# Performance work log

Measured on AMD Instinct MI355X. Metric: run time of the kernel, lower is better.

The kernel has to match this reference:

```python
import jax, jax.numpy as jnp
import numpy as np

SINGLE_DIM = 256
PAIR_DIM = 64
MAX_REL_POS = 32
LN_EPS = 1e-5


def setup_inputs() -> dict:
    key = jax.random.key(0)
    ks = jax.random.split(key, 6)
    B, N = 2, 1024
    single_repr = jax.random.normal(ks[0], (B, N, SINGLE_DIM), dtype=jnp.float32)
    # Linear(single_dim*2 -> pair_dim)
    lim = 1.0 / np.sqrt(2 * SINGLE_DIM)
    W = jax.random.uniform(ks[1], (2 * SINGLE_DIM, PAIR_DIM), minval=-lim, maxval=lim, dtype=jnp.float32)
    b = jax.random.uniform(ks[2], (PAIR_DIM,), minval=-lim, maxval=lim, dtype=jnp.float32)
    # LayerNorm(pair_dim)
    gamma = jnp.ones((PAIR_DIM,), dtype=jnp.float32)
    beta = jnp.zeros((PAIR_DIM,), dtype=jnp.float32)
    # Embedding(2*max_rel_pos+1, pair_dim)
    embed = jax.random.normal(ks[3], (2 * MAX_REL_POS + 1, PAIR_DIM), dtype=jnp.float32)
    return {"single_repr": single_repr, "W": W, "b": b, "gamma": gamma, "beta": beta, "embed": embed}


def reference(single_repr, W, b, gamma, beta, embed):
    B, N, d = single_repr.shape
    # Split the Linear weight: cat([s_i, s_j]) @ W == s_i @ W_i + s_j @ W_j.
    # This avoids materializing the [B,N,N,2d] concat tensor (outer-sum trick).
    W_i, W_j = W[:d], W[d:]                       # [d, pair_dim] each
    proj_i = jnp.einsum('bnd,dp->bnp', single_repr, W_i)  # [B,N,P]
    proj_j = jnp.einsum('bnd,dp->bnp', single_repr, W_j)  # [B,N,P]
    x = proj_i[:, :, None, :] + proj_j[:, None, :, :] + b  # [B,N,N,P]
    # LayerNorm over last dim
    mu = jnp.mean(x, axis=-1, keepdims=True)
    var = jnp.mean((x - mu) ** 2, axis=-1, keepdims=True)
    x = (x - mu) * jax.lax.rsqrt(var + LN_EPS) * gamma + beta
    x = jax.nn.relu(x)
    # Relative position embedding
    pos = jnp.arange(N)
    rel = jnp.clip(pos[None, :] - pos[:, None], -MAX_REL_POS, MAX_REL_POS) + MAX_REL_POS  # [N,N]
    x = x + embed[rel][None]  # broadcast over batch
    return x
```

## Files before the change

### kernel.cpp

```cpp
#include <hip/hip_runtime.h>

#define SINGLE_DIM 256
#define PAIR_DIM   64
#define MAX_REL    32
#define LN_EPS     1e-5f
#define N_FIXED    1024

__global__ __launch_bounds__(128) void proj_kernel(
    const float* __restrict__ s,
    const float* __restrict__ W,
    const float* __restrict__ bias,
    float* __restrict__ proj)
{
    __shared__ float lds[4][SINGLE_DIM];
    const int row0 = blockIdx.x * 4;
    const int t = threadIdx.x;

    {
        const float4* src = (const float4*)(s + (size_t)row0 * SINGLE_DIM);
        float4* dst = (float4*)(&lds[0][0]);
        dst[t]       = src[t];
        dst[t + 128] = src[t + 128];
    }
    __syncthreads();

    const int c4   = (t & 31) * 4;
    const int row  = t >> 5;
    const int half = c4 >> 6;
    const int p0   = c4 & 63;
    const float* Wbase = W + half * (SINGLE_DIM * PAIR_DIM) + p0;
    const float* srow  = lds[row];

    float4 acc = {0.f, 0.f, 0.f, 0.f};
    #pragma unroll
    for (int d = 0; d < SINGLE_DIM; d += 4) {
        float4 s4 = *(const float4*)(srow + d);
        float4 w0 = *(const float4*)(Wbase + (d + 0) * PAIR_DIM);
        float4 w1 = *(const float4*)(Wbase + (d + 1) * PAIR_DIM);
        float4 w2 = *(const float4*)(Wbase + (d + 2) * PAIR_DIM);
        float4 w3 = *(const float4*)(Wbase + (d + 3) * PAIR_DIM);
        acc.x += s4.x * w0.x; acc.y += s4.x * w0.y; acc.z += s4.x * w0.z; acc.w += s4.x * w0.w;
        acc.x += s4.y * w1.x; acc.y += s4.y * w1.y; acc.z += s4.y * w1.z; acc.w += s4.y * w1.w;
        acc.x += s4.z * w2.x; acc.y += s4.z * w2.y; acc.z += s4.z * w2.z; acc.w += s4.z * w2.w;
        acc.x += s4.w * w3.x; acc.y += s4.w * w3.y; acc.z += s4.w * w3.z; acc.w += s4.w * w3.w;
    }
    if (half == 0) {
        float4 b4 = *(const float4*)(bias + p0);
        acc.x += b4.x; acc.y += b4.y; acc.z += b4.z; acc.w += b4.w;
    }
    *(float4*)(proj + (size_t)(row0 + row) * 128 + c4) = acc;
}

__global__ __launch_bounds__(256) void pair_kernel(
    const float* __restrict__ proj,
    const float* __restrict__ gamma,
    const float* __restrict__ beta,
    const float* __restrict__ embed,
    float* __restrict__ out)
{
    const int t = threadIdx.x;
    const int pairIdx = blockIdx.x * 16 + (t >> 4);
    const int p0 = (t & 15) * 4;

    const int j  = pairIdx & (N_FIXED - 1);
    const int bi = pairIdx >> 10;
    const int i  = bi & (N_FIXED - 1);
    const int b  = bi >> 10;

    const float4 pi4 = *(const float4*)(proj + (size_t)bi * 128 + p0);
    const float4 pj4 = *(const float4*)(proj + (size_t)(b * N_FIXED + j) * 128 + 64 + p0);

    float4 v;
    v.x = pi4.x + pj4.x;
    v.y = pi4.y + pj4.y;
    v.z = pi4.z + pj4.z;
    v.w = pi4.w + pj4.w;

    float s  = v.x + v.y + v.z + v.w;
    float ss = v.x * v.x + v.y * v.y + v.z * v.z + v.w * v.w;
    #pragma unroll
    for (int mask = 1; mask < 16; mask <<= 1) {
        s  += __shfl_xor(s,  mask, 64);
        ss += __shfl_xor(ss, mask, 64);
    }
    const float mean = s * (1.f / PAIR_DIM);
    const float var  = ss * (1.f / PAIR_DIM) - mean * mean;
    const float rstd = rsqrtf(var + LN_EPS);

    const float4 g4 = *(const float4*)(gamma + p0);
    const float4 b4 = *(const float4*)(beta + p0);

    int rel = j - i;
    rel = (rel < -MAX_REL) ? -MAX_REL : (rel > MAX_REL ? MAX_REL : rel);
    rel += MAX_REL;
    const float4 e4 = *(const float4*)(embed + rel * PAIR_DIM + p0);

    float4 o;
    o.x = fmaxf((v.x - mean) * rstd * g4.x + b4.x, 0.f) + e4.x;
    o.y = fmaxf((v.y - mean) * rstd * g4.y + b4.y, 0.f) + e4.y;
    o.z = fmaxf((v.z - mean) * rstd * g4.z + b4.z, 0.f) + e4.z;
    o.w = fmaxf((v.w - mean) * rstd * g4.w + b4.w, 0.f) + e4.w;

    *(float4*)(out + (size_t)pairIdx * PAIR_DIM + p0) = o;
}

extern "C" void kernel_launch(void* const* d_in, const int* in_sizes, int n_in,
                              void* d_out, int out_size, void* d_ws, size_t ws_size,
                              hipStream_t stream) {
    const float* s     = (const float*)d_in[0];
    const float* W     = (const float*)d_in[1];
    const float* bias  = (const float*)d_in[2];
    const float* gamma = (const float*)d_in[3];
    const float* beta  = (const float*)d_in[4];
    const float* embed = (const float*)d_in[5];
    float* out  = (float*)d_out;
    float* proj = (float*)d_ws;

    const int BN = in_sizes[0] / SINGLE_DIM;

    proj_kernel<<<BN / 4, 128, 0, stream>>>(s, W, bias, proj);

    const int pairs = BN * N_FIXED;
    pair_kernel<<<pairs / 16, 256, 0, stream>>>(proj, gamma, beta, embed, out);
}
```

Measured before the change: 575.0 us.

## Process four pairs per thread group, use nontemporal stores, simplify projection kernel

Result: faster. 539.6 us (-6.2%).

```diff
diff --git a/kernel.cpp b/kernel.cpp
--- a/kernel.cpp
+++ b/kernel.cpp
@@ -6,49 +6,35 @@
 #define LN_EPS     1e-5f
 #define N_FIXED    1024
 
-__global__ __launch_bounds__(128) void proj_kernel(
+typedef float vfloat4 __attribute__((ext_vector_type(4)));
+
+__global__ __launch_bounds__(256) void proj_kernel(
     const float* __restrict__ s,
     const float* __restrict__ W,
     const float* __restrict__ bias,
     float* __restrict__ proj)
 {
-    __shared__ float lds[4][SINGLE_DIM];
-    const int row0 = blockIdx.x * 4;
+    __shared__ float lds[2][SINGLE_DIM];
+    const int row0 = blockIdx.x * 2;
     const int t = threadIdx.x;
 
-    {
-        const float4* src = (const float4*)(s + (size_t)row0 * SINGLE_DIM);
-        float4* dst = (float4*)(&lds[0][0]);
-        dst[t]       = src[t];
-        dst[t + 128] = src[t + 128];
-    }
+    ((float2*)(&lds[0][0]))[t] = ((const float2*)(s + (size_t)row0 * SINGLE_DIM))[t];
     __syncthreads();
 
-    const int c4   = (t & 31) * 4;
-    const int row  = t >> 5;
-    const int half = c4 >> 6;
-    const int p0   = c4 & 63;
-    const float* Wbase = W + half * (SINGLE_DIM * PAIR_DIM) + p0;
-    const float* srow  = lds[row];
+    const int row  = t >> 7;
+    const int c    = t & 127;
+    const int half = c >> 6;
+    const int p    = c & 63;
 
-    float4 acc = {0.f, 0.f, 0.f, 0.f};
-    #pragma unroll
-    for (int d = 0; d < SINGLE_DIM; d += 4) {
-        float4 s4 = *(const float4*)(srow + d);
-        float4 w0 = *(const float4*)(Wbase + (d + 0) * PAIR_DIM);
-        float4 w1 = *(const float4*)(Wbase + (d + 1) * PAIR_DIM);
-        float4 w2 = *(const float4*)(Wbase + (d + 2) * PAIR_DIM);
-        float4 w3 = *(const float4*)(Wbase + (d + 3) * PAIR_DIM);
-        acc.x += s4.x * w0.x; acc.y += s4.x * w0.y; acc.z += s4.x * w0.z; acc.w += s4.x * w0.w;
-        acc.x += s4.y * w1.x; acc.y += s4.y * w1.y; acc.z += s4.y * w1.z; acc.w += s4.y * w1.w;
-        acc.x += s4.z * w2.x; acc.y += s4.z * w2.y; acc.z += s4.z * w2.z; acc.w += s4.z * w2.w;
-        acc.x += s4.w * w3.x; acc.y += s4.w * w3.y; acc.z += s4.w * w3.z; acc.w += s4.w * w3.w;
-    }
-    if (half == 0) {
-        float4 b4 = *(const float4*)(bias + p0);
-        acc.x += b4.x; acc.y += b4.y; acc.z += b4.z; acc.w += b4.w;
-    }
-    *(float4*)(proj + (size_t)(row0 + row) * 128 + c4) = acc;
+    const float* wcol = W + half * (SINGLE_DIM * PAIR_DIM) + p;
+    const float* srow = lds[row];
+
+    float acc = (half == 0) ? bias[p] : 0.f;
+    #pragma unroll 8
+    for (int d = 0; d < SINGLE_DIM; ++d)
+        acc += srow[d] * wcol[d * PAIR_DIM];
+
+    proj[(size_t)(row0 + row) * 128 + c] = acc;
 }
 
 __global__ __launch_bounds__(256) void pair_kernel(
@@ -58,50 +44,63 @@
     const float* __restrict__ embed,
     float* __restrict__ out)
 {
-    const int t = threadIdx.x;
-    const int pairIdx = blockIdx.x * 16 + (t >> 4);
+    const int t  = threadIdx.x;
+    const int g  = t >> 4;
     const int p0 = (t & 15) * 4;
-
-    const int j  = pairIdx & (N_FIXED - 1);
-    const int bi = pairIdx >> 10;
-    const int i  = bi & (N_FIXED - 1);
-    const int b  = bi >> 10;
+    const int bid = blockIdx.x;
+    const int bi    = bid >> 4;
+    const int jbase = (bid & 15) * 64 + g;
+    const int i = bi & (N_FIXED - 1);
+    const int b = bi >> 10;
 
     const float4 pi4 = *(const float4*)(proj + (size_t)bi * 128 + p0);
-    const float4 pj4 = *(const float4*)(proj + (size_t)(b * N_FIXED + j) * 128 + 64 + p0);
+    const float4 g4  = *(const float4*)(gamma + p0);
+    const float4 b4  = *(const float4*)(beta + p0);
 
-    float4 v;
-    v.x = pi4.x + pj4.x;
-    v.y = pi4.y + pj4.y;
-    v.z = pi4.z + pj4.z;
-    v.w = pi4.w + pj4.w;
+    float4 v[4];
+    float  s[4], ss[4];
+    #pragma unroll
+    for (int k = 0; k < 4; ++k) {
+        const int j = jbase + 16 * k;
+        const float4 pj4 = *(const float4*)(proj + (size_t)(b * N_FIXED + j) * 128 + 64 + p0);
+        v[k].x = pi4.x + pj4.x;
+        v[k].y = pi4.y + pj4.y;
+        v[k].z = pi4.z + pj4.z;
+        v[k].w = pi4.w + pj4.w;
+        s[k]  = v[k].x + v[k].y + v[k].z + v[k].w;
+        ss[k] = v[k].x * v[k].x + v[k].y * v[k].y + v[k].z * v[k].z + v[k].w * v[k].w;
+    }
 
-    float s  = v.x + v.y + v.z + v.w;
-    float ss = v.x * v.x + v.y * v.y + v.z * v.z + v.w * v.w;
     #pragma unroll
     for (int mask = 1; mask < 16; mask <<= 1) {
-        s  += __shfl_xor(s,  mask, 64);
-        ss += __shfl_xor(ss, mask, 64);
+        #pragma unroll
+        for (int k = 0; k < 4; ++k) {
+            s[k]  += __shfl_xor(s[k],  mask, 64);
+            ss[k] += __shfl_xor(ss[k], mask, 64);
+        }
     }
-    const float mean = s * (1.f / PAIR_DIM);
-    const float var  = ss * (1.f / PAIR_DIM) - mean * mean;
-    const float rstd = rsqrtf(var + LN_EPS);
 
-    const float4 g4 = *(const float4*)(gamma + p0);
-    const float4 b4 = *(const float4*)(beta + p0);
+    #pragma unroll
+    for (int k = 0; k < 4; ++k) {
+        const int j = jbase + 16 * k;
+        const float mean = s[k] * (1.f / PAIR_DIM);
+        const float var  = ss[k] * (1.f / PAIR_DIM) - mean * mean;
+        const float rstd = rsqrtf(var + LN_EPS);
 
-    int rel = j - i;
-    rel = (rel < -MAX_REL) ? -MAX_REL : (rel > MAX_REL ? MAX_REL : rel);
-    rel += MAX_REL;
-    const float4 e4 = *(const float4*)(embed + rel * PAIR_DIM + p0);
+        int rel = j - i;
+        rel = (rel < -MAX_REL) ? -MAX_REL : (rel > MAX_REL ? MAX_REL : rel);
+        rel += MAX_REL;
+        const float4 e4 = *(const float4*)(embed + rel * PAIR_DIM + p0);
 
-    float4 o;
-    o.x = fmaxf((v.x - mean) * rstd * g4.x + b4.x, 0.f) + e4.x;
-    o.y = fmaxf((v.y - mean) * rstd * g4.y + b4.y, 0.f) + e4.y;
-    o.z = fmaxf((v.z - mean) * rstd * g4.z + b4.z, 0.f) + e4.z;
-    o.w = fmaxf((v.w - mean) * rstd * g4.w + b4.w, 0.f) + e4.w;
+        vfloat4 o;
+        o.x = fmaxf((v[k].x - mean) * rstd * g4.x + b4.x, 0.f) + e4.x;
+        o.y = fmaxf((v[k].y - mean) * rstd * g4.y + b4.y, 0.f) + e4.y;
+        o.z = fmaxf((v[k].z - mean) * rstd * g4.z + b4.z, 0.f) + e4.z;
+        o.w = fmaxf((v[k].w - mean) * rstd * g4.w + b4.w, 0.f) + e4.w;
 
-    *(float4*)(out + (size_t)pairIdx * PAIR_DIM + p0) = o;
+        __builtin_nontemporal_store(o,
+            (vfloat4*)(out + ((size_t)bi * N_FIXED + j) * PAIR_DIM + p0));
+    }
 }
 
 extern "C" void kernel_launch(void* const* d_in, const int* in_sizes, int n_in,
@@ -118,8 +117,8 @@
 
     const int BN = in_sizes[0] / SINGLE_DIM;
 
-    proj_kernel<<<BN / 4, 128, 0, stream>>>(s, W, bias, proj);
+    proj_kernel<<<BN / 2, 256, 0, stream>>>(s, W, bias, proj);
 
-    const int pairs = BN * N_FIXED;
-    pair_kernel<<<pairs / 16, 256, 0, stream>>>(proj, gamma, beta, embed, out);
+    const int blocks = BN * (N_FIXED / 64);
+    pair_kernel<<<blocks, 256, 0, stream>>>(proj, gamma, beta, embed, out);
 }
```
